# Kernel optimization log

Hardware: AMD Instinct MI355X
Metric: run time of the kernel (lower is better)

The kernel has to match this reference:

```python
import jax, jax.numpy as jnp
import numpy as np
from jax import lax

D_MODEL = 1024
D_INNER = 2 * D_MODEL  # expand=2
D_CONV = 4
BATCH = 4
SEQ = 4096


def setup_inputs() -> dict:
    key = jax.random.key(0)
    ks = jax.random.split(key, 10)
    s = 0.02
    return {
        "x": jax.random.normal(ks[0], (BATCH, SEQ, D_MODEL), jnp.float32),
        "in_proj_w": jax.random.normal(ks[1], (2 * D_INNER, D_MODEL), jnp.float32) * s,
        "in_proj_b": jnp.zeros((2 * D_INNER,), jnp.float32),
        "conv_w": jax.random.normal(ks[2], (D_INNER, 1, D_CONV), jnp.float32) * s,
        "conv_b": jnp.zeros((D_INNER,), jnp.float32),
        "dt_w": jax.random.normal(ks[3], (D_INNER, D_INNER), jnp.float32) * s,
        "dt_b": jnp.zeros((D_INNER,), jnp.float32),
        "b_w": jax.random.normal(ks[4], (D_INNER, D_INNER), jnp.float32) * s,
        "c_w": jax.random.normal(ks[5], (D_INNER, D_INNER), jnp.float32) * s,
        "A_log": jax.random.normal(ks[6], (D_INNER,), jnp.float32) * 0.02 - 2.0,
        "D_param": jnp.ones((D_INNER,), jnp.float32),
        "out_w": jax.random.normal(ks[7], (D_MODEL, D_INNER), jnp.float32) * s,
        "out_b": jnp.zeros((D_MODEL,), jnp.float32),
    }


def _mixer(x, in_proj_w, in_proj_b, conv_w, conv_b, dt_w, dt_b,
           b_w, c_w, A_log, D_param, out_w, out_b):
    B, L, _ = x.shape
    # input projection -> split into x/z branches
    xz = jnp.einsum("bld,ed->ble", x, in_proj_w) + in_proj_b
    x_branch, z_branch = jnp.split(xz, 2, axis=-1)  # each [B, L, d_inner]

    # causal depthwise conv1d (padding=d_conv-1 on the left == torch pad then [:L])
    u = jnp.transpose(x_branch, (0, 2, 1))  # [B, d_inner, L]
    u = lax.conv_general_dilated(
        u, conv_w,
        window_strides=(1,),
        padding=[(D_CONV - 1, 0)],
        dimension_numbers=("NCH", "OIH", "NCH"),
        feature_group_count=D_INNER,
    ) + conv_b[None, :, None]
    u = jnp.transpose(u, (0, 2, 1))  # [B, L, d_inner]
    u = jax.nn.silu(u)

    dt = jax.nn.softplus(jnp.einsum("bld,ed->ble", u, dt_w) + dt_b) + 1e-4
    B_t = jnp.tanh(jnp.einsum("bld,ed->ble", u, b_w))
    C_t = jnp.tanh(jnp.einsum("bld,ed->ble", u, c_w))

    A = jnp.exp(A_log)  # [d_inner]
    decay = jnp.exp(-dt * A)          # [B, L, d_inner]
    inc = (1.0 - decay) * B_t * u     # [B, L, d_inner]

    # linear recurrence: state_t = decay_t * state_{t-1} + inc_t
    def step(state, xs):
        d_t, i_t = xs
        state = d_t * state + i_t
        return state, state

    init = jnp.zeros((B, D_INNER), x.dtype)
    _, states = lax.scan(step, init,
                         (jnp.transpose(decay, (1, 0, 2)),
                          jnp.transpose(inc, (1, 0, 2))))  # [L, B, d_inner]
    states = jnp.transpose(states, (1, 0, 2))  # [B, L, d_inner]

    y = C_t * states + D_param * u
    y = y * jax.nn.sigmoid(z_branch)  # SiLU-style gate
    # dropout is identity in eval mode
    return jnp.einsum("ble,de->bld", y, out_w) + out_b


def reference(x, in_proj_w, in_proj_b, conv_w, conv_b, dt_w, dt_b,
              b_w, c_w, A_log, D_param, out_w, out_b):
    return _mixer(x, in_proj_w, in_proj_b, conv_w, conv_b, dt_w, dt_b,
                  b_w, c_w, A_log, D_param, out_w, out_b)
```

## Files before the change

### kernel.cpp

```cpp
#include <hip/hip_runtime.h>
#include <math.h>
#include <stdint.h>


#define BATCH 4
#define SEQ 4096
#define DMODEL 1024
#define DINNER 2048
#define CLS 32

typedef __bf16 bf16_t;
typedef __bf16 bf16x8 __attribute__((ext_vector_type(8)));
typedef float f32x4 __attribute__((ext_vector_type(4)));
typedef unsigned short ushort_t;
typedef unsigned short u16x4 __attribute__((ext_vector_type(4)));

enum { EP_F32 = 0, EP_BF = 1, EP_DBC = 2, EP_GATE = 3 };

__device__ __forceinline__ void gload_lds16(const void* g, void* l) {
    __builtin_amdgcn_global_load_lds(
        (const __attribute__((address_space(1))) void*)g,
        (__attribute__((address_space(3))) void*)l, 16, 0, 0);
}

__device__ __forceinline__ ushort_t f2bf(float f) {
    union { float f; uint32_t u; } c; c.f = f;
    uint32_t u = c.u;
    u += 0x7fffu + ((u >> 16) & 1u);
    return (ushort_t)(u >> 16);
}
__device__ __forceinline__ float bf2f(ushort_t h) {
    union { uint32_t u; float f; } c; c.u = (uint32_t)h << 16;
    return c.f;
}
__device__ __forceinline__ float tanh_exact(float v) {
    v = fminf(fmaxf(v, -15.f), 15.f);
    float e = __expf(2.f * v);
    return (e - 1.f) / (e + 1.f);
}
__device__ __forceinline__ float tanh_poly(float v) {
    float v2 = v * v;
    float t = v * (1.f - v2 * (0.33333333f - 0.13333333f * v2));
    if (__builtin_expect(fabsf(v) > 0.25f, 0)) t = tanh_exact(v);
    return t;
}
__device__ __forceinline__ float softplus_poly(float v) {
    float v2 = v * v;
    float s = 0.69314718f + 0.5f * v + v2 * (0.125f - 0.0052083333f * v2);
    if (__builtin_expect(fabsf(v) > 0.25f, 0))
        s = fmaxf(v, 0.f) + __logf(1.f + __expf(-fabsf(v)));
    return s;
}

#define WAITV2 asm volatile("s_waitcnt vmcnt(2)" ::: "memory")
#define WAITV0 asm volatile("s_waitcnt vmcnt(0)" ::: "memory")

__global__ __launch_bounds__(512) void gemm256_ep(
    const bf16_t* __restrict__ A, const bf16_t* __restrict__ W,
    const float* __restrict__ bias, float* __restrict__ Cf,
    ushort_t* __restrict__ T0, ushort_t* __restrict__ T1,
    ushort_t* __restrict__ T2, const float* __restrict__ alogp,
    int K, int Nout, int Lc, int a_bstride, int a_l0,
    int c_bstride, int c_l0, int mode)
{
    __shared__ __align__(16) char smem[131072];
    const int tid = threadIdx.x;
    const int lane = tid & 63;
    const int wid = tid >> 6;
    const int wm2 = wid >> 2;
    const int wn2 = wid & 3;
    const int wz = blockIdx.z;
    const bf16_t* Wmat = W + (size_t)wz * Nout * K;
    ushort_t* Tz = (wz == 0) ? T0 : (wz == 1 ? T1 : T2);
    const int n0 = blockIdx.x * 256;
    const int m0 = blockIdx.y * 256;
    const int bb = m0 / Lc;
    const int lb = m0 - bb * Lc;
    const bf16_t* Abase = A + ((size_t)bb * a_bstride + a_l0 + lb) * K;
    const bf16_t* Wbase = Wmat + (size_t)n0 * K;

    int r_[2], c_[2], lofs_[2];
#pragma unroll
    for (int i = 0; i < 2; ++i) {
        int ofs = tid * 16 + i * 8192;
        int r = ofs >> 7;
        int c16 = (ofs >> 4) & 7;
        r_[i] = r;
        c_[i] = (c16 ^ (r & 7)) << 3;
        lofs_[i] = ofs;
    }

    const int nt = K / 64;

    f32x4 acc[4][4][2];
#pragma unroll
    for (int q = 0; q < 4; ++q)
#pragma unroll
        for (int mi = 0; mi < 4; ++mi)
#pragma unroll
            for (int ni = 0; ni < 2; ++ni) acc[q][mi][ni] = f32x4{0.f, 0.f, 0.f, 0.f};

#pragma unroll
    for (int s = 0; s < 4; ++s) {
        const int isB_ = (s == 1 || s == 2);
        const int h_ = (s >= 2) ? 1 : 0;
        char* dst_ = smem + (isB_ ? 32768 : 0) + h_ * 16384;
        const bf16_t* g_ = isB_ ? Wbase : Abase;
        gload_lds16(g_ + (size_t)(h_ * 128 + r_[0]) * K + c_[0], dst_ + lofs_[0]);
        gload_lds16(g_ + (size_t)(h_ * 128 + r_[1]) * K + c_[1], dst_ + lofs_[1]);
    }

#define STAGE(S)                                                              \
    if (t + 1 < nt) {                                                         \
      char* base_ = smem + (((t + 1) & 1) ? 65536 : 0);                       \
      const int isB_ = ((S) == 1 || (S) == 2);                                \
      const int h_ = ((S) >= 2) ? 1 : 0;                                      \
      char* dst_ = base_ + (isB_ ? 32768 : 0) + h_ * 16384;                   \
      const bf16_t* g_ = isB_ ? Wbase : Abase;                                \
      const int k0_ = (t + 1) * 64;                                           \
      gload_lds16(g_ + (size_t)(h_ * 128 + r_[0]) * K + k0_ + c_[0],          \
                  dst_ + lofs_[0]);                                           \
      gload_lds16(g_ + (size_t)(h_ * 128 + r_[1]) * K + k0_ + c_[1],          \
                  dst_ + lofs_[1]);                                           \
    }

#define READ_A(dst, half)                                                     \
    _Pragma("unroll") for (int mi = 0; mi < 4; ++mi)                          \
    _Pragma("unroll") for (int ks = 0; ks < 2; ++ks) {                        \
      int row = (half) * 128 + wm2 * 64 + mi * 16 + (lane & 15);              \
      int cb = (ks * 64 + ((lane >> 4) << 4)) ^ ((row & 7) << 4);             \
      dst[mi][ks] = *(const bf16x8*)(bufb + row * 128 + cb);                  \
    }

#define READ_B(dst, half)                                                     \
    _Pragma("unroll") for (int ni = 0; ni < 2; ++ni)                          \
    _Pragma("unroll") for (int ks = 0; ks < 2; ++ks) {                        \
      int row = (half) * 128 + wn2 * 32 + ni * 16 + (lane & 15);              \
      int cb = (ks * 64 + ((lane >> 4) << 4)) ^ ((row & 7) << 4);             \
      dst[ni][ks] = *(const bf16x8*)(bufb + 32768 + row * 128 + cb);          \
    }

#define MMA(Q, AV, BV)                                                        \
    __builtin_amdgcn_s_setprio(1);                                            \
    _Pragma("unroll") for (int ks = 0; ks < 2; ++ks)                          \
    _Pragma("unroll") for (int mi = 0; mi < 4; ++mi)                          \
    _Pragma("unroll") for (int ni = 0; ni < 2; ++ni)                          \
      acc[(Q)][mi][ni] = __builtin_amdgcn_mfma_f32_16x16x32_bf16(             \
          AV[mi][ks], BV[ni][ks], acc[(Q)][mi][ni], 0, 0, 0);                 \
    __builtin_amdgcn_s_setprio(0);

    for (int t = 0; t < nt; ++t) {
        const char* bufb = smem + ((t & 1) ? 65536 : 0);
        bf16x8 av0[4][2], av1[4][2], bv0[2][2], bv1[2][2];
        STAGE(0)
        if (t + 1 < nt) { WAITV2; } else { WAITV0; }
        __builtin_amdgcn_s_barrier();
        READ_A(av0, 0)
        READ_B(bv0, 0)
        READ_B(bv1, 1)
        READ_A(av1, 1)
        MMA(0, av0, bv0)
        STAGE(1)
        MMA(1, av0, bv1)
        STAGE(2)
        MMA(3, av1, bv1)
        STAGE(3)
        MMA(2, av1, bv0)
        __builtin_amdgcn_s_barrier();
    }
#undef STAGE
#undef READ_A
#undef READ_B
#undef MMA

    __syncthreads();

    const size_t rowbase = (size_t)bb * c_bstride + c_l0 + lb;
    if (mode == EP_F32) {
#pragma unroll
        for (int q = 0; q < 4; ++q) {
#pragma unroll
            for (int ni = 0; ni < 2; ++ni) {
                const int col = (q & 1) * 128 + wn2 * 32 + ni * 16 + (lane & 15);
                const float bv = bias ? bias[n0 + col] : 0.f;
#pragma unroll
                for (int mi = 0; mi < 4; ++mi) {
#pragma unroll
                    for (int r4 = 0; r4 < 4; ++r4) {
                        const int row = (q >> 1) * 128 + wm2 * 64 + mi * 16 +
                                        ((lane >> 4) << 2) + r4;
                        Cf[(rowbase + row) * (size_t)Nout + n0 + col] =
                            acc[q][mi][ni][r4] + bv;
                    }
                }
            }
        }
        return;
    }

    ushort_t* sm = (ushort_t*)smem;
#pragma unroll
    for (int q = 0; q < 4; ++q) {
#pragma unroll
        for (int ni = 0; ni < 2; ++ni) {
            const int col = (q & 1) * 128 + wn2 * 32 + ni * 16 + (lane & 15);
            float bv = 0.f, Ae = 0.f;
            if (mode == EP_BF || mode == EP_GATE) bv = bias[n0 + col];
            else if (mode == EP_DBC && wz == 0) {
                bv = bias[n0 + col]; Ae = __expf(alogp[n0 + col]);
            }
#pragma unroll
            for (int mi = 0; mi < 4; ++mi) {
#pragma unroll
                for (int r4 = 0; r4 < 4; ++r4) {
                    const int row = (q >> 1) * 128 + wm2 * 64 + mi * 16 +
                                    ((lane >> 4) << 2) + r4;
                    float v = acc[q][mi][ni][r4] + bv;
                    ushort_t o;
                    if (mode == EP_BF) {
                        o = f2bf(v);
                    } else if (mode == EP_GATE) {
                        const size_t off = (rowbase + row) * (size_t)Nout + n0 + col;
                        o = f2bf(bf2f(Tz[off]) / (1.f + __expf(-v)));
                    } else {
                        if (wz == 0)
                            o = f2bf(__expf(-(softplus_poly(v) + 1e-4f) * Ae));
                        else
                            o = f2bf(tanh_poly(v));
                    }
                    const int sbyte = row * 512 + (((col * 2) ^ ((row & 7) << 4)));
                    *(ushort_t*)((char*)sm + sbyte) = o;
                }
            }
        }
    }
    __syncthreads();
#pragma unroll
    for (int it = 0; it < 16; ++it) {
        const int b0 = tid * 16 + it * 8192;
        const int row = b0 >> 9;
        const int inrow = b0 & 511;
        const int src = row * 512 + (inrow ^ ((row & 7) << 4));
        int4 vv = *(const int4*)((const char*)sm + src);
        *(int4*)(Tz + (rowbase + row) * (size_t)Nout + n0 + (inrow >> 1)) = vv;
    }
}

__global__ __launch_bounds__(256) void cvt_bf16_k(
    const float4* __restrict__ in, ushort4* __restrict__ out, int n4)
{
    for (int i = blockIdx.x * 256 + threadIdx.x; i < n4; i += gridDim.x * 256) {
        float4 v = in[i];
        ushort4 o;
        o.x = f2bf(v.x); o.y = f2bf(v.y); o.z = f2bf(v.z); o.w = f2bf(v.w);
        out[i] = o;
    }
}

__global__ __launch_bounds__(256) void conv_silu_bf(
    const ushort_t* __restrict__ xb, const ushort_t* __restrict__ tailb,
    const float* __restrict__ cw, const float* __restrict__ cb,
    ushort_t* __restrict__ ubf, int Lc, int l0, size_t total)
{
    for (size_t idx = (size_t)blockIdx.x * 256 + threadIdx.x; idx < total;
         idx += (size_t)gridDim.x * 256) {
        int e = (int)(idx % DINNER);
        size_t r = idx / DINNER;
        int lp = (int)(r % Lc);
        int b  = (int)(r / Lc);
        float4 w = *(const float4*)(cw + (size_t)e * 4);
        float s = cb[e];
        const ushort_t* xbase = xb + (size_t)b * Lc * DINNER + e;
        if (lp >= 3) {
            s += bf2f(xbase[(size_t)(lp - 3) * DINNER]) * w.x
               + bf2f(xbase[(size_t)(lp - 2) * DINNER]) * w.y
               + bf2f(xbase[(size_t)(lp - 1) * DINNER]) * w.z
               + bf2f(xbase[(size_t)lp * DINNER]) * w.w;
        } else {
            const float ws4[4] = {w.x, w.y, w.z, w.w};
            const ushort_t* tbase = tailb + (size_t)b * 3 * DINNER + e;
#pragma unroll
            for (int j = 0; j < 4; ++j) {
                int ls = lp - 3 + j;
                float v;
                if (ls >= 0)            v = bf2f(xbase[(size_t)ls * DINNER]);
                else if (l0 + ls >= 0)  v = bf2f(tbase[(size_t)(3 + ls) * DINNER]);
                else                    v = 0.f;
                s += v * ws4[j];
            }
        }
        ubf[idx] = f2bf(s / (1.f + __expf(-s)));
    }
}

__global__ __launch_bounds__(256) void tail_update_bf(
    const ushort_t* __restrict__ xb, ushort_t* __restrict__ tailb, int Lc)
{
    int idx = blockIdx.x * 256 + threadIdx.x;
    if (idx >= BATCH * 3 * DINNER) return;
    int e = idx % DINNER;
    int j = (idx / DINNER) % 3;
    int b = idx / (3 * DINNER);
    tailb[idx] = xb[((size_t)b * Lc + Lc - 3 + j) * DINNER + e];
}

__global__ __launch_bounds__(256) void scan1_v4(
    const ushort_t* __restrict__ dec, const ushort_t* __restrict__ bt,
    const ushort_t* __restrict__ ub,
    float* __restrict__ P, float* __restrict__ S, int Lc, int nsub)
{
    int t = blockIdx.x * 256 + threadIdx.x;
    int e = (t & 511) << 2;
    int rest = t >> 9;
    int c = rest % nsub;
    int b = rest / nsub;
    size_t off = ((size_t)b * Lc + (size_t)c * CLS) * DINNER + e;
    float p[4] = {1.f, 1.f, 1.f, 1.f};
    float s[4] = {0.f, 0.f, 0.f, 0.f};
    for (int t0 = 0; t0 < CLS; ++t0) {
        size_t o = off + (size_t)t0 * DINNER;
        u16x4 d4 = *(const u16x4*)(dec + o);
        u16x4 b4 = *(const u16x4*)(bt + o);
        u16x4 u4 = *(const u16x4*)(ub + o);
#pragma unroll
        for (int j = 0; j < 4; ++j) {
            float d = bf2f(d4[j]);
            float inc = (1.f - d) * bf2f(b4[j]) * bf2f(u4[j]);
            s[j] = d * s[j] + inc;
            p[j] *= d;
        }
    }
    size_t po = ((size_t)b * nsub + c) * DINNER + e;
    *(float4*)(P + po) = float4{p[0], p[1], p[2], p[3]};
    *(float4*)(S + po) = float4{s[0], s[1], s[2], s[3]};
}

__global__ __launch_bounds__(256) void scan_p2(
    float* __restrict__ P, float* __restrict__ S,
    float* __restrict__ carry, int nsub, int first)
{
    int idx = blockIdx.x * 256 + threadIdx.x;
    int e = idx % DINNER;
    int b = idx / DINNER;
    float cv = first ? 0.f : carry[idx];
    for (int c = 0; c < nsub; ++c) {
        size_t o = ((size_t)b * nsub + c) * DINNER + e;
        float p = P[o], s = S[o];
        P[o] = cv;
        cv = p * cv + s;
    }
    carry[idx] = cv;
}

__global__ __launch_bounds__(256) void p3y_v4(
    const ushort_t* __restrict__ dec, ushort_t* __restrict__ bty,
    const ushort_t* __restrict__ ct, const ushort_t* __restrict__ ub,
    const float* __restrict__ Dp, const float* __restrict__ Pc,
    int Lc, int nsub)
{
    int t = blockIdx.x * 256 + threadIdx.x;
    int e = (t & 511) << 2;
    int rest = t >> 9;
    int c = rest % nsub;
    int b = rest / nsub;
    size_t off = ((size_t)b * Lc + (size_t)c * CLS) * DINNER + e;
    size_t po = ((size_t)b * nsub + c) * DINNER + e;
    float4 stv = *(const float4*)(Pc + po);
    float4 Dv  = *(const float4*)(Dp + e);
    float st[4] = {stv.x, stv.y, stv.z, stv.w};
    float D4[4] = {Dv.x, Dv.y, Dv.z, Dv.w};
    for (int t0 = 0; t0 < CLS; ++t0) {
        size_t o = off + (size_t)t0 * DINNER;
        u16x4 d4 = *(const u16x4*)(dec + o);
        u16x4 b4 = *(const u16x4*)(bty + o);
        u16x4 c4 = *(const u16x4*)(ct + o);
        u16x4 u4 = *(const u16x4*)(ub + o);
        u16x4 y4;
#pragma unroll
        for (int j = 0; j < 4; ++j) {
            float d = bf2f(d4[j]);
            float u = bf2f(u4[j]);
            float inc = (1.f - d) * bf2f(b4[j]) * u;
            st[j] = d * st[j] + inc;
            y4[j] = f2bf(bf2f(c4[j]) * st[j] + D4[j] * u);
        }
        *(u16x4*)(bty + o) = y4;
    }
}

extern "C" void kernel_launch(void* const* d_in, const int* in_sizes, int n_in,
                              void* d_out, int out_size, void* d_ws, size_t ws_size,
                              hipStream_t stream)
{
    const float* x    = (const float*)d_in[0];
    const float* ipw  = (const float*)d_in[1];
    const float* ipb  = (const float*)d_in[2];
    const float* cw   = (const float*)d_in[3];
    const float* cb   = (const float*)d_in[4];
    const float* dtw  = (const float*)d_in[5];
    const float* dtb  = (const float*)d_in[6];
    const float* bw   = (const float*)d_in[7];
    const float* cwt  = (const float*)d_in[8];
    const float* alog = (const float*)d_in[9];
    const float* dpar = (const float*)d_in[10];
    const float* ow   = (const float*)d_in[11];
    const float* ob   = (const float*)d_in[12];
    float* out = (float*)d_out;

    const size_t XN   = (size_t)BATCH * SEQ * DMODEL;
    const size_t WIP  = (size_t)2 * DINNER * DMODEL;
    const size_t WSQ  = (size_t)DINNER * DINNER;
    const size_t WOUT = (size_t)DMODEL * DINNER;
    const size_t const_bytes = 2 * (XN + WIP + 3 * WSQ + WOUT);

    const int cands[5] = {4096, 2048, 1024, 512, 256};
    int Lc = 256;
    for (int i = 0; i < 5; ++i) {
        size_t NBe = (size_t)BATCH * cands[i] * DINNER;
        size_t need = const_bytes
                    + 4 * NBe * 2
                    + (size_t)BATCH * 3 * DINNER * 2
                    + (size_t)BATCH * DINNER * 4
                    + 2 * (size_t)BATCH * (cands[i] / CLS) * DINNER * 4
                    + 1024;
        if (need <= ws_size) { Lc = cands[i]; break; }
    }
    const int nsub = Lc / CLS;
    const size_t NBe = (size_t)BATCH * Lc * DINNER;

    char* p = (char*)d_ws;
    ushort_t* xbf   = (ushort_t*)p; p += XN * 2;
    ushort_t* ipwbf = (ushort_t*)p; p += WIP * 2;
    ushort_t* wcat  = (ushort_t*)p; p += 3 * WSQ * 2;
    ushort_t* owbf  = (ushort_t*)p; p += WOUT * 2;
    ushort_t* S1 = (ushort_t*)p; p += NBe * 2;
    ushort_t* S2 = (ushort_t*)p; p += NBe * 2;
    ushort_t* S3 = (ushort_t*)p; p += NBe * 2;
    ushort_t* S4 = (ushort_t*)p; p += NBe * 2;
    ushort_t* tailb = (ushort_t*)p; p += (size_t)BATCH * 3 * DINNER * 2;
    float* carry = (float*)p; p += (size_t)BATCH * DINNER * 4;
    float* Pb    = (float*)p; p += (size_t)BATCH * nsub * DINNER * 4;
    float* Sb    = (float*)p;

    const dim3 blk(256);
    const dim3 blk512(512);
    const int M = BATCH * Lc;
    const dim3 g256(DINNER / 256, M / 256, 1);
    const dim3 g256z3(DINNER / 256, M / 256, 3);
    const dim3 g256out(DMODEL / 256, M / 256, 1);
    const int pwBlocks = (int)(((NBe + 255) / 256 < 4096) ? (NBe + 255) / 256 : 4096);
    const int scanBlocks = BATCH * nsub * 2;

    auto cvt = [&](const float* in, ushort_t* outp, size_t n) {
        int n4 = (int)(n / 4);
        int g = n4 / 256 < 2048 ? (n4 + 255) / 256 : 2048;
        cvt_bf16_k<<<g, blk, 0, stream>>>((const float4*)in, (ushort4*)outp, n4);
    };
    cvt(x, xbf, XN);
    cvt(ipw, ipwbf, WIP);
    cvt(dtw, wcat, WSQ);
    cvt(bw, wcat + WSQ, WSQ);
    cvt(cwt, wcat + 2 * WSQ, WSQ);
    cvt(ow, owbf, WOUT);

    const int nchunks = SEQ / Lc;
    for (int c = 0; c < nchunks; ++c) {
        const int l0 = c * Lc;
        gemm256_ep<<<g256, blk512, 0, stream>>>(
            (const bf16_t*)xbf, (const bf16_t*)ipwbf, ipb,
            nullptr, S1, nullptr, nullptr, nullptr,
            DMODEL, DINNER, Lc, SEQ, l0, Lc, 0, EP_BF);
        conv_silu_bf<<<pwBlocks, blk, 0, stream>>>(S1, tailb, cw, cb, S2, Lc, l0, NBe);
        if (nchunks > 1)
            tail_update_bf<<<BATCH * 3 * DINNER / 256, blk, 0, stream>>>(S1, tailb, Lc);
        gemm256_ep<<<g256z3, blk512, 0, stream>>>(
            (const bf16_t*)S2, (const bf16_t*)wcat, dtb,
            nullptr, S3, S4, S1, alog,
            DINNER, DINNER, Lc, Lc, 0, Lc, 0, EP_DBC);
        scan1_v4<<<scanBlocks, blk, 0, stream>>>(S3, S4, S2, Pb, Sb, Lc, nsub);
        scan_p2<<<BATCH * DINNER / 256, blk, 0, stream>>>(Pb, Sb, carry, nsub, c == 0);
        p3y_v4<<<scanBlocks, blk, 0, stream>>>(S3, S4, S1, S2, dpar, Pb, Lc, nsub);
        gemm256_ep<<<g256, blk512, 0, stream>>>(
            (const bf16_t*)xbf, (const bf16_t*)(ipwbf + (size_t)DINNER * DMODEL),
            ipb + DINNER, nullptr, S4, nullptr, nullptr, nullptr,
            DMODEL, DINNER, Lc, SEQ, l0, Lc, 0, EP_GATE);
        gemm256_ep<<<g256out, blk512, 0, stream>>>(
            (const bf16_t*)S4, (const bf16_t*)owbf, ob,
            out, nullptr, nullptr, nullptr, nullptr,
            DINNER, DMODEL, Lc, Lc, 0, SEQ, l0, EP_F32);
    }
}
```

Baseline: 1.025 ms.

## Merge x/z projection GEMMs into one launch and apply gate in scan output

The x and z halves of the input projection now run as a single GEMM launch with grid z=2. The z half stores sigmoid(z) to a new bf16 buffer, and the gating multiply moves into the scan output kernel, replacing the separate gate GEMM that had to re-read y. The GEMM main loop also reorders its LDS fragment reads, adding lgkmcnt waits and sched barriers so that reads for later MMAs are issued after earlier MMAs start. The cost is one extra full-size bf16 intermediate buffer (more workspace and memory traffic), plus the risk that the explicit waits serialize LDS reads against MFMA.

```diff
diff --git a/kernel.cpp b/kernel.cpp
--- a/kernel.cpp
+++ b/kernel.cpp
@@ -15,7 +15,7 @@
 typedef unsigned short ushort_t;
 typedef unsigned short u16x4 __attribute__((ext_vector_type(4)));
 
-enum { EP_F32 = 0, EP_BF = 1, EP_DBC = 2, EP_GATE = 3 };
+enum { EP_XZ = 0, EP_DBC = 1, EP_F32 = 2 };
 
 __device__ __forceinline__ void gload_lds16(const void* g, void* l) {
     __builtin_amdgcn_global_load_lds(
@@ -54,6 +54,7 @@
 
 #define WAITV2 asm volatile("s_waitcnt vmcnt(2)" ::: "memory")
 #define WAITV0 asm volatile("s_waitcnt vmcnt(0)" ::: "memory")
+#define WAITL0 asm volatile("s_waitcnt lgkmcnt(0)" ::: "memory")
 
 __global__ __launch_bounds__(512) void gemm256_ep(
     const bf16_t* __restrict__ A, const bf16_t* __restrict__ W,
@@ -157,12 +158,15 @@
         __builtin_amdgcn_s_barrier();
         READ_A(av0, 0)
         READ_B(bv0, 0)
-        READ_B(bv1, 1)
-        READ_A(av1, 1)
+        WAITL0; __builtin_amdgcn_sched_barrier(0);
         MMA(0, av0, bv0)
         STAGE(1)
+        READ_B(bv1, 1)
+        WAITL0; __builtin_amdgcn_sched_barrier(0);
         MMA(1, av0, bv1)
         STAGE(2)
+        READ_A(av1, 1)
+        WAITL0; __builtin_amdgcn_sched_barrier(0);
         MMA(3, av1, bv1)
         STAGE(3)
         MMA(2, av1, bv0)
@@ -205,8 +209,9 @@
         for (int ni = 0; ni < 2; ++ni) {
             const int col = (q & 1) * 128 + wn2 * 32 + ni * 16 + (lane & 15);
             float bv = 0.f, Ae = 0.f;
-            if (mode == EP_BF || mode == EP_GATE) bv = bias[n0 + col];
-            else if (mode == EP_DBC && wz == 0) {
+            if (mode == EP_XZ) {
+                bv = bias[wz * Nout + n0 + col];
+            } else if (wz == 0) {
                 bv = bias[n0 + col]; Ae = __expf(alogp[n0 + col]);
             }
 #pragma unroll
@@ -217,11 +222,9 @@
                                     ((lane >> 4) << 2) + r4;
                     float v = acc[q][mi][ni][r4] + bv;
                     ushort_t o;
-                    if (mode == EP_BF) {
-                        o = f2bf(v);
-                    } else if (mode == EP_GATE) {
-                        const size_t off = (rowbase + row) * (size_t)Nout + n0 + col;
-                        o = f2bf(bf2f(Tz[off]) / (1.f + __expf(-v)));
+                    if (mode == EP_XZ) {
+                        o = (wz == 0) ? f2bf(v)
+                                      : f2bf(1.f / (1.f + __expf(-v)));
                     } else {
                         if (wz == 0)
                             o = f2bf(__expf(-(softplus_poly(v) + 1e-4f) * Ae));
@@ -355,8 +358,8 @@
 __global__ __launch_bounds__(256) void p3y_v4(
     const ushort_t* __restrict__ dec, ushort_t* __restrict__ bty,
     const ushort_t* __restrict__ ct, const ushort_t* __restrict__ ub,
-    const float* __restrict__ Dp, const float* __restrict__ Pc,
-    int Lc, int nsub)
+    const ushort_t* __restrict__ sg, const float* __restrict__ Dp,
+    const float* __restrict__ Pc, int Lc, int nsub)
 {
     int t = blockIdx.x * 256 + threadIdx.x;
     int e = (t & 511) << 2;
@@ -375,6 +378,7 @@
         u16x4 b4 = *(const u16x4*)(bty + o);
         u16x4 c4 = *(const u16x4*)(ct + o);
         u16x4 u4 = *(const u16x4*)(ub + o);
+        u16x4 g4 = *(const u16x4*)(sg + o);
         u16x4 y4;
 #pragma unroll
         for (int j = 0; j < 4; ++j) {
@@ -382,7 +386,8 @@
             float u = bf2f(u4[j]);
             float inc = (1.f - d) * bf2f(b4[j]) * u;
             st[j] = d * st[j] + inc;
-            y4[j] = f2bf(bf2f(c4[j]) * st[j] + D4[j] * u);
+            float y = bf2f(c4[j]) * st[j] + D4[j] * u;
+            y4[j] = f2bf(y * bf2f(g4[j]));
         }
         *(u16x4*)(bty + o) = y4;
     }
@@ -418,7 +423,7 @@
     for (int i = 0; i < 5; ++i) {
         size_t NBe = (size_t)BATCH * cands[i] * DINNER;
         size_t need = const_bytes
-                    + 4 * NBe * 2
+                    + 5 * NBe * 2
                     + (size_t)BATCH * 3 * DINNER * 2
                     + (size_t)BATCH * DINNER * 4
                     + 2 * (size_t)BATCH * (cands[i] / CLS) * DINNER * 4
@@ -437,6 +442,7 @@
     ushort_t* S2 = (ushort_t*)p; p += NBe * 2;
     ushort_t* S3 = (ushort_t*)p; p += NBe * 2;
     ushort_t* S4 = (ushort_t*)p; p += NBe * 2;
+    ushort_t* S5 = (ushort_t*)p; p += NBe * 2;
     ushort_t* tailb = (ushort_t*)p; p += (size_t)BATCH * 3 * DINNER * 2;
     float* carry = (float*)p; p += (size_t)BATCH * DINNER * 4;
     float* Pb    = (float*)p; p += (size_t)BATCH * nsub * DINNER * 4;
@@ -445,9 +451,9 @@
     const dim3 blk(256);
     const dim3 blk512(512);
     const int M = BATCH * Lc;
-    const dim3 g256(DINNER / 256, M / 256, 1);
-    const dim3 g256z3(DINNER / 256, M / 256, 3);
-    const dim3 g256out(DMODEL / 256, M / 256, 1);
+    const dim3 gXZ(DINNER / 256, M / 256, 2);
+    const dim3 gDBC(DINNER / 256, M / 256, 3);
+    const dim3 gOut(DMODEL / 256, M / 256, 1);
     const int pwBlocks = (int)(((NBe + 255) / 256 < 4096) ? (NBe + 255) / 256 : 4096);
     const int scanBlocks = BATCH * nsub * 2;
 
@@ -466,27 +472,23 @@
     const int nchunks = SEQ / Lc;
     for (int c = 0; c < nchunks; ++c) {
         const int l0 = c * Lc;
-        gemm256_ep<<<g256, blk512, 0, stream>>>(
-            (const bf16_t*)xbf, (const bf16_t*)ipwbf, ipb,
-            nullptr, S1, nullptr, nullptr, nullptr,
-            DMODEL, DINNER, Lc, SEQ, l0, Lc, 0, EP_BF);
+        gemm256_ep<<<gXZ, blk512, 0, stream>>>(
+            (const bf16_t*)xbf, (const bf16_t*)ipwbf, ipb, nullptr,
+            S1, S5, nullptr, nullptr,
+            DMODEL, DINNER, Lc, SEQ, l0, Lc, 0, EP_XZ);
         conv_silu_bf<<<pwBlocks, blk, 0, stream>>>(S1, tailb, cw, cb, S2, Lc, l0, NBe);
         if (nchunks > 1)
             tail_update_bf<<<BATCH * 3 * DINNER / 256, blk, 0, stream>>>(S1, tailb, Lc);
-        gemm256_ep<<<g256z3, blk512, 0, stream>>>(
-            (const bf16_t*)S2, (const bf16_t*)wcat, dtb,
-            nullptr, S3, S4, S1, alog,
+        gemm256_ep<<<gDBC, blk512, 0, stream>>>(
+            (const bf16_t*)S2, (const bf16_t*)wcat, dtb, nullptr,
+            S3, S4, S1, alog,
             DINNER, DINNER, Lc, Lc, 0, Lc, 0, EP_DBC);
         scan1_v4<<<scanBlocks, blk, 0, stream>>>(S3, S4, S2, Pb, Sb, Lc, nsub);
         scan_p2<<<BATCH * DINNER / 256, blk, 0, stream>>>(Pb, Sb, carry, nsub, c == 0);
-        p3y_v4<<<scanBlocks, blk, 0, stream>>>(S3, S4, S1, S2, dpar, Pb, Lc, nsub);
-        gemm256_ep<<<g256, blk512, 0, stream>>>(
-            (const bf16_t*)xbf, (const bf16_t*)(ipwbf + (size_t)DINNER * DMODEL),
-            ipb + DINNER, nullptr, S4, nullptr, nullptr, nullptr,
-            DMODEL, DINNER, Lc, SEQ, l0, Lc, 0, EP_GATE);
-        gemm256_ep<<<g256out, blk512, 0, stream>>>(
-            (const bf16_t*)S4, (const bf16_t*)owbf, ob,
-            out, nullptr, nullptr, nullptr, nullptr,
+        p3y_v4<<<scanBlocks, blk, 0, stream>>>(S3, S4, S1, S2, S5, dpar, Pb, Lc, nsub);
+        gemm256_ep<<<gOut, blk512, 0, stream>>>(
+            (const bf16_t*)S4, (const bf16_t*)owbf, ob, out,
+            nullptr, nullptr, nullptr, nullptr,
             DINNER, DMODEL, Lc, Lc, 0, SEQ, l0, EP_F32);
     }
 }
```

After: 917.9 us. 1.12x faster.
